# Optimization experiments

Hardware: AMD Instinct MI355X
Metric: run time of the kernel (lower is better)

Reference implementation:

```python
import jax, jax.numpy as jnp
import numpy as np
from functools import partial

NPOINT, NSAMPLE = 1024, 32
EPS = 1e-5

def setup_inputs() -> dict:
    key = jax.random.key(0)
    ks = jax.random.split(key, 16)
    B, N, C = 16, 4096, 64
    d = {
        "xyz": jax.random.normal(ks[0], (B, N, 3), jnp.float32),
        "points": jax.random.normal(ks[1], (B, N, C), jnp.float32),
    }
    chans = [67, 64, 64, 128]
    for i in range(3):
        cin, cout = chans[i], chans[i + 1]
        d[f"w{i+1}"] = jax.random.normal(ks[2 + i], (cout, cin), jnp.float32) * (1.0 / np.sqrt(cin))
        d[f"b{i+1}"] = jnp.zeros((cout,), jnp.float32)
        d[f"g{i+1}"] = jnp.ones((cout,), jnp.float32)
        d[f"be{i+1}"] = jnp.zeros((cout,), jnp.float32)
    return d

def farthest_point_sample(xyz, npoint):
    # xyz: (B, N, 3); deterministic start index 0 (torch code uses randint)
    B, N, _ = xyz.shape
    bidx = jnp.arange(B)

    def step(carry, _):
        distance, farthest = carry
        centroid = xyz[bidx, farthest]                       # (B, 3)
        dist = jnp.sum((xyz - centroid[:, None, :]) ** 2, -1)  # (B, N)
        distance = jnp.minimum(distance, dist)
        return (distance, jnp.argmax(distance, axis=1)), farthest

    init = (jnp.full((B, N), 1e10, xyz.dtype), jnp.zeros((B,), jnp.int32))
    _, centroids = jax.lax.scan(step, init, None, length=npoint)  # (npoint, B)
    return centroids.T                                            # (B, npoint)

def knn_group(nsample, xyz, new_xyz, points):
    # xyz: (B,N,3), new_xyz: (B,S,3), points: (B,N,C)
    # squared distances (same topk ordering as cdist)
    d2 = (jnp.sum(new_xyz ** 2, -1)[:, :, None]
          + jnp.sum(xyz ** 2, -1)[:, None, :]
          - 2.0 * jnp.einsum("bsd,bnd->bsn", new_xyz, xyz))     # (B,S,N)
    _, idx = jax.lax.top_k(-d2, nsample)                          # (B,S,K)

    gather = jax.vmap(lambda feats, i: feats[i])                  # per-batch fancy index
    grouped_xyz = gather(xyz, idx) - new_xyz[:, :, None, :]       # (B,S,K,3)
    grouped_pts = jnp.concatenate([grouped_xyz, gather(points, idx)], -1)  # (B,S,K,3+C)
    return grouped_xyz, grouped_pts

def mlp_layer(x, w, b, g, be):
    # 1x1 conv + BatchNorm (batch stats, training mode) + ReLU
    y = jnp.einsum("bskc,oc->bsko", x, w) + b
    mu = jnp.mean(y, axis=(0, 1, 2))
    var = jnp.var(y, axis=(0, 1, 2))
    y = (y - mu) * jax.lax.rsqrt(var + EPS) * g + be
    return jax.nn.relu(y)

def reference(xyz, points, w1, b1, g1, be1, w2, b2, g2, be2, w3, b3, g3, be3):
    centroids = farthest_point_sample(xyz, NPOINT)                    # (B,S)
    new_xyz = jnp.take_along_axis(xyz, centroids[:, :, None], axis=1)  # (B,S,3)
    _, x = knn_group(NSAMPLE, xyz, new_xyz, points)                   # (B,S,K,3+C)
    x = mlp_layer(x, w1, b1, g1, be1)
    x = mlp_layer(x, w2, b2, g2, be2)
    x = mlp_layer(x, w3, b3, g3, be3)
    new_points = jnp.max(x, axis=2)                                   # (B,S,mlp[-1])
    return new_xyz, new_points
```

## Files before the change

kernel.cpp:

```cpp
#include <hip/hip_runtime.h>

typedef unsigned int   uint;
typedef unsigned short ushort;
typedef unsigned long long u64;
typedef float f32x4 __attribute__((ext_vector_type(4)));
typedef short bf16x8 __attribute__((ext_vector_type(8)));
typedef uint  uint2v __attribute__((ext_vector_type(2)));

#define STR  88
#define STR1 104

__device__ __forceinline__ uint packbf2(float a, float b){
  uint ua=__float_as_uint(a); ua=(ua+0x7fffu+((ua>>16)&1u))>>16;
  uint ub=__float_as_uint(b); ub=(ub+0x7fffu+((ub>>16)&1u))>>16;
  return ua|(ub<<16);
}
__device__ __forceinline__ ushort bf1(float a){
  uint ua=__float_as_uint(a); return (ushort)((ua+0x7fffu+((ua>>16)&1u))>>16);
}

__global__ __launch_bounds__(256) void k_fps(const float* __restrict__ xyz,
                                             int* __restrict__ cent,
                                             float* __restrict__ oxyz,
                                             float* __restrict__ pxyz){
  __shared__ __align__(16) float sp[4096][4];
  __shared__ u64 rk[2][4];
  __shared__ int sel[1024];
  const int b = blockIdx.x, tid = threadIdx.x, lane=tid&63, wave=tid>>6;
  const float* xb = xyz + (long)b*4096*3;
  float px[16], py[16], pz[16], pd[16];
#pragma unroll
  for (int j=0;j<16;j++){
    int n = tid + 256*j;
    float x=xb[n*3], y=xb[n*3+1], z=xb[n*3+2];
    sp[n][0]=x; sp[n][1]=y; sp[n][2]=z; sp[n][3]=0.0f;
    px[j]=x; py[j]=y; pz[j]=z; pd[j]=1e10f;
  }
  if (tid==0) sel[0]=0;
  __syncthreads();
  int f = 0;
  for (int t=1;t<1024;t++){
    f32x4 c = *(const f32x4*)sp[f];
    float bv=-1.0f; int bi=0;
#pragma unroll
    for (int j=0;j<16;j++){
      int n = tid + 256*j;
      float dx=px[j]-c[0], dy=py[j]-c[1], dz=pz[j]-c[2];
      float d=__fadd_rn(__fadd_rn(__fmul_rn(dx,dx),__fmul_rn(dy,dy)),__fmul_rn(dz,dz));
      float mn=fminf(pd[j],d); pd[j]=mn;
      if (j==0){ bv=mn; bi=n; }
      else if (mn>bv){ bv=mn; bi=n; }
    }
    u64 key = ((u64)__float_as_uint(bv)<<32) | (uint)(~bi);
#pragma unroll
    for (int off=32;off;off>>=1){
      u64 ok=__shfl_xor(key,off);
      key = ok>key ? ok : key;
    }
    int par=t&1;
    if (lane==0) rk[par][wave]=key;
    __syncthreads();
    {
      u64 k0=rk[par][0], k1=rk[par][1], k2=rk[par][2], k3=rk[par][3];
      u64 ka = k0>k1?k0:k1;
      u64 kb = k2>k3?k2:k3;
      u64 kk = ka>kb?ka:kb;
      f = (int)(~(uint)kk) & 4095;
    }
    if (tid==0) sel[t]=f;
  }
  __syncthreads();
#pragma unroll
  for (int j=0;j<4;j++){
    int s = tid + 256*j;
    int n = sel[s];
    cent[b*1024+s]=n;
    f32x4 cf=*(const f32x4*)sp[n];
    oxyz[(b*1024+s)*3+0]=cf[0];
    oxyz[(b*1024+s)*3+1]=cf[1];
    oxyz[(b*1024+s)*3+2]=cf[2];
  }
#pragma unroll
  for (int j=0;j<16;j++){
    int n = tid + 256*j;
    *(f32x4*)(pxyz + ((long)b*4096+n)*4) = *(const f32x4*)sp[n];
  }
}

__global__ __launch_bounds__(256) void k_knn(const float* __restrict__ pxyz,
                                             const int* __restrict__ cent,
                                             ushort* __restrict__ kidx){
  const int bx=blockIdx.x, b=bx>>6, hc=bx&63;
  const int tid=threadIdx.x, lane=tid&63, wave=tid>>6;
  const f32x4* __restrict__ P = (const f32x4*)pxyz + (long)b*4096;
  const u64 SENT=~0ull;
  for (int qp=0; qp<2; qp++){
    int sA = hc*16 + wave*4 + qp*2;
    int sB = sA + 1;
    int qnA = cent[b*1024 + sA] & 4095;
    int qnB = cent[b*1024 + sB] & 4095;
    f32x4 QA = P[qnA], QB = P[qnB];
    double qxA=(double)QA[0], qyA=(double)QA[1], qzA=(double)QA[2];
    double qxB=(double)QB[0], qyB=(double)QB[1], qzB=(double)QB[2];
    u64 k1A=SENT, k2A=SENT, k1B=SENT, k2B=SENT;
#pragma unroll 4
    for (int j=0;j<64;j++){
      int n = lane + 64*j;
      f32x4 pt = P[n];
      double px=(double)pt[0], py=(double)pt[1], pz=(double)pt[2];
      double dxA=px-qxA, dyA=py-qyA, dzA=pz-qzA;
      double dxB=px-qxB, dyB=py-qyB, dzB=pz-qzB;
      double d2A = dxA*dxA + dyA*dyA + dzA*dzA;
      double d2B = dxB*dxB + dyB*dyB + dzB*dzB;
      u64 kdA = (((u64)__double_as_longlong(d2A)) & ~4095ull) | (uint)n;
      u64 kdB = (((u64)__double_as_longlong(d2B)) & ~4095ull) | (uint)n;
      if (kdA<k1A){ k2A=k1A; k1A=kdA; }
      else if (kdA<k2A){ k2A=kdA; }
      if (kdB<k1B){ k2B=k1B; k1B=kdB; }
      else if (kdB<k2B){ k2B=kdB; }
    }
    u64 removedA=0ull, removedB=0ull;
    ushort* outA = kidx + (b*1024 + sA)*32;
    ushort* outB = kidx + (b*1024 + sB)*32;
    for (int r=0;r<32;r++){
      u64 wkA=k1A, wkB=k1B;
#pragma unroll
      for (int off=32;off;off>>=1){
        u64 okA=__shfl_xor(wkA,off);
        u64 okB=__shfl_xor(wkB,off);
        wkA = okA<wkA ? okA : wkA;
        wkB = okB<wkB ? okB : wkB;
      }
      if (lane==0){ outA[r]=(ushort)(wkA & 4095u); outB[r]=(ushort)(wkB & 4095u); }
      if (wkA==k1A){
        removedA |= 1ull << (((uint)(k1A&4095u))>>6);
        if (k2A!=SENT){ k1A=k2A; k2A=SENT; }
        else {
          k1A=SENT; k2A=SENT;
#pragma unroll 4
          for (int j=0;j<64;j++){
            if ((removedA>>j)&1ull) continue;
            int n = lane + 64*j;
            f32x4 pt = P[n];
            double dx=(double)pt[0]-qxA, dy=(double)pt[1]-qyA, dz=(double)pt[2]-qzA;
            double d2 = dx*dx + dy*dy + dz*dz;
            u64 kd = (((u64)__double_as_longlong(d2)) & ~4095ull) | (uint)n;
            if (kd<k1A){ k2A=k1A; k1A=kd; }
            else if (kd<k2A){ k2A=kd; }
          }
        }
      }
      if (wkB==k1B){
        removedB |= 1ull << (((uint)(k1B&4095u))>>6);
        if (k2B!=SENT){ k1B=k2B; k2B=SENT; }
        else {
          k1B=SENT; k2B=SENT;
#pragma unroll 4
          for (int j=0;j<64;j++){
            if ((removedB>>j)&1ull) continue;
            int n = lane + 64*j;
            f32x4 pt = P[n];
            double dx=(double)pt[0]-qxB, dy=(double)pt[1]-qyB, dz=(double)pt[2]-qzB;
            double d2 = dx*dx + dy*dy + dz*dz;
            u64 kd = (((u64)__double_as_longlong(d2)) & ~4095ull) | (uint)n;
            if (kd<k1B){ k2B=k1B; k1B=kd; }
            else if (kd<k2B){ k2B=kd; }
          }
        }
      }
    }
  }
}

__global__ __launch_bounds__(256) void k_mlp1m(const float* __restrict__ xyz,
                                               const float* __restrict__ pts,
                                               const float* __restrict__ w1,
                                               const float* __restrict__ b1,
                                               const int* __restrict__ cent,
                                               const ushort* __restrict__ kidx,
                                               float* __restrict__ part,
                                               float* __restrict__ y){
  __shared__ __align__(16) ushort SA[128*STR1];
  __shared__ __align__(16) ushort SW[64*STR1];
  __shared__ float WRED[4*4*16*2];
  const int tid=threadIdx.x, bi=blockIdx.x;
  const int lane=tid&63, wave=tid>>6;
  const int lo16=lane&15, hi16=lane>>4;
  const long bN=(long)(bi>>6)*4096;

  for (int i=tid;i<64*96;i+=256){
    int r=i/96, c=i-r*96;
    float v = (c<64)? w1[r*67+3+c] : (c<67? w1[r*67+(c-64)] : 0.0f);
    SW[r*STR1+c]=bf1(v);
  }
  for (int i=tid;i<128*32;i+=256){
    int r=i>>5, c=64+(i&31);
    SA[r*STR1+c]=0;
  }
  const int ch4=(tid&15)*4, rb=(tid>>4)*8;
  float a1r[4];
#pragma unroll
  for (int nf=0;nf<4;nf++) a1r[nf]=b1[nf*16+lo16];
  float pss[4]={0.f,0.f,0.f,0.f}, pqq[4]={0.f,0.f,0.f,0.f};

  for (int t=0;t<4;t++){
    const long row0=(long)bi*512 + t*128;
    __syncthreads();
#pragma unroll
    for(int rr=0;rr<8;rr++){
      int r=rb+rr;
      long grow=row0+r;
      int n = kidx[grow] & 4095;
      f32x4 v=*(const f32x4*)(pts + (bN+n)*64 + ch4);
      uint2v pk; pk[0]=packbf2(v[0],v[1]); pk[1]=packbf2(v[2],v[3]);
      *(uint2v*)(SA+r*STR1+ch4)=pk;
    }
    if (tid<128){
      int r=tid;
      long grow=row0+r;
      int n = kidx[grow] & 4095;
      int q = cent[grow>>5] & 4095;
      const float* xp = xyz + (bN+n)*3;
      const float* qp = xyz + (bN+q)*3;
      SA[r*STR1+64]=bf1(xp[0]-qp[0]);
      SA[r*STR1+65]=bf1(xp[1]-qp[1]);
      SA[r*STR1+66]=bf1(xp[2]-qp[2]);
    }
    __syncthreads();
    const int mt=wave*32;
    f32x4 acc[2][4];
#pragma unroll
    for(int mf=0;mf<2;mf++)
#pragma unroll
      for(int nf=0;nf<4;nf++) acc[mf][nf]=(f32x4){0.f,0.f,0.f,0.f};
#pragma unroll
    for (int ks=0; ks<3; ks++){
      bf16x8 a0=*(const bf16x8*)(SA+(mt+lo16)*STR1    + ks*32 + hi16*8);
      bf16x8 a1f=*(const bf16x8*)(SA+(mt+16+lo16)*STR1 + ks*32 + hi16*8);
      bf16x8 b0=*(const bf16x8*)(SW+(lo16)*STR1     + ks*32 + hi16*8);
      bf16x8 b1f=*(const bf16x8*)(SW+(16+lo16)*STR1 + ks*32 + hi16*8);
      bf16x8 b2f=*(const bf16x8*)(SW+(32+lo16)*STR1 + ks*32 + hi16*8);
      bf16x8 b3f=*(const bf16x8*)(SW+(48+lo16)*STR1 + ks*32 + hi16*8);
      acc[0][0]=__builtin_amdgcn_mfma_f32_16x16x32_bf16(a0 ,b0 ,acc[0][0],0,0,0);
      acc[0][1]=__builtin_amdgcn_mfma_f32_16x16x32_bf16(a0 ,b1f,acc[0][1],0,0,0);
      acc[0][2]=__builtin_amdgcn_mfma_f32_16x16x32_bf16(a0 ,b2f,acc[0][2],0,0,0);
      acc[0][3]=__builtin_amdgcn_mfma_f32_16x16x32_bf16(a0 ,b3f,acc[0][3],0,0,0);
      acc[1][0]=__builtin_amdgcn_mfma_f32_16x16x32_bf16(a1f,b0 ,acc[1][0],0,0,0);
      acc[1][1]=__builtin_amdgcn_mfma_f32_16x16x32_bf16(a1f,b1f,acc[1][1],0,0,0);
      acc[1][2]=__builtin_amdgcn_mfma_f32_16x16x32_bf16(a1f,b2f,acc[1][2],0,0,0);
      acc[1][3]=__builtin_amdgcn_mfma_f32_16x16x32_bf16(a1f,b3f,acc[1][3],0,0,0);
    }
#pragma unroll
    for (int nf=0;nf<4;nf++){
#pragma unroll
      for (int mf=0;mf<2;mf++)
#pragma unroll
        for (int reg=0;reg<4;reg++){
          float d=acc[mf][nf][reg]+a1r[nf];
          long rr=row0+mt+mf*16+hi16*4+reg;
          y[rr*64 + nf*16+lo16]=d;
          pss[nf]+=d; pqq[nf]=fmaf(d,d,pqq[nf]);
        }
    }
  }
#pragma unroll
  for (int nf=0;nf<4;nf++){
    pss[nf]+=__shfl_xor(pss[nf],16); pss[nf]+=__shfl_xor(pss[nf],32);
    pqq[nf]+=__shfl_xor(pqq[nf],16); pqq[nf]+=__shfl_xor(pqq[nf],32);
  }
  if (lane<16){
#pragma unroll
    for (int nf=0;nf<4;nf++){
      WRED[((wave*4+nf)*16+lane)*2+0]=pss[nf];
      WRED[((wave*4+nf)*16+lane)*2+1]=pqq[nf];
    }
  }
  __syncthreads();
  if (tid<64){
    int ch=tid, nf=ch>>4, ci=ch&15;
    float s=0.f,q=0.f;
#pragma unroll
    for (int w=0;w<4;w++){ s+=WRED[((w*4+nf)*16+ci)*2]; q+=WRED[((w*4+nf)*16+ci)*2+1]; }
    part[(bi*64+ch)*2]=s; part[(bi*64+ch)*2+1]=q;
  }
}

__global__ __launch_bounds__(256) void k_mlp2m(const float* __restrict__ w2,
                                               const float* __restrict__ b2,
                                               const float* __restrict__ ab1,
                                               float* __restrict__ part,
                                               float* __restrict__ y){
  __shared__ __align__(16) ushort SA[128*STR];
  __shared__ __align__(16) ushort SW[64*STR];
  __shared__ float WRED[4*4*16*2];
  const int tid=threadIdx.x, bi=blockIdx.x;
  const int lane=tid&63, wave=tid>>6;
  const int lo16=lane&15, hi16=lane>>4;

  for (int i=tid;i<4096;i+=256){
    int r=i>>6, c=i&63;
    SW[r*STR+c]=bf1(w2[i]);
  }
  const int ch4=(tid&15)*4, rb=(tid>>4)*8;
  float a1[4],c1[4];
#pragma unroll
  for(int j=0;j<4;j++){ a1[j]=ab1[(ch4+j)*2]; c1[j]=ab1[(ch4+j)*2+1]; }
  float bbn[4];
#pragma unroll
  for (int nf=0;nf<4;nf++) bbn[nf]=b2[nf*16+lo16];
  float pss[4]={0.f,0.f,0.f,0.f}, pqq[4]={0.f,0.f,0.f,0.f};

  for (int t=0;t<4;t++){
    const long row0=(long)bi*512 + t*128;
    __syncthreads();
#pragma unroll
    for(int rr=0;rr<8;rr++){
      int r=rb+rr;
      f32x4 v=*(const f32x4*)(y+(row0+r)*64+ch4);
      float x0=fmaxf(fmaf(a1[0],v[0],c1[0]),0.f);
      float x1=fmaxf(fmaf(a1[1],v[1],c1[1]),0.f);
      float x2=fmaxf(fmaf(a1[2],v[2],c1[2]),0.f);
      float x3=fmaxf(fmaf(a1[3],v[3],c1[3]),0.f);
      uint2v pk; pk[0]=packbf2(x0,x1); pk[1]=packbf2(x2,x3);
      *(uint2v*)(SA+r*STR+ch4)=pk;
    }
    __syncthreads();
    const int mt=wave*32;
    f32x4 acc[2][4];
#pragma unroll
    for(int mf=0;mf<2;mf++)
#pragma unroll
      for(int nf=0;nf<4;nf++) acc[mf][nf]=(f32x4){0.f,0.f,0.f,0.f};
#pragma unroll
    for (int ks=0; ks<2; ks++){
      bf16x8 a0=*(const bf16x8*)(SA+(mt+lo16)*STR    + ks*32 + hi16*8);
      bf16x8 a1f=*(const bf16x8*)(SA+(mt+16+lo16)*STR + ks*32 + hi16*8);
      bf16x8 b0=*(const bf16x8*)(SW+(lo16)*STR     + ks*32 + hi16*8);
      bf16x8 b1=*(const bf16x8*)(SW+(16+lo16)*STR  + ks*32 + hi16*8);
      bf16x8 b2f=*(const bf16x8*)(SW+(32+lo16)*STR + ks*32 + hi16*8);
      bf16x8 b3f=*(const bf16x8*)(SW+(48+lo16)*STR + ks*32 + hi16*8);
      acc[0][0]=__builtin_amdgcn_mfma_f32_16x16x32_bf16(a0 ,b0 ,acc[0][0],0,0,0);
      acc[0][1]=__builtin_amdgcn_mfma_f32_16x16x32_bf16(a0 ,b1 ,acc[0][1],0,0,0);
      acc[0][2]=__builtin_amdgcn_mfma_f32_16x16x32_bf16(a0 ,b2f,acc[0][2],0,0,0);
      acc[0][3]=__builtin_amdgcn_mfma_f32_16x16x32_bf16(a0 ,b3f,acc[0][3],0,0,0);
      acc[1][0]=__builtin_amdgcn_mfma_f32_16x16x32_bf16(a1f,b0 ,acc[1][0],0,0,0);
      acc[1][1]=__builtin_amdgcn_mfma_f32_16x16x32_bf16(a1f,b1 ,acc[1][1],0,0,0);
      acc[1][2]=__builtin_amdgcn_mfma_f32_16x16x32_bf16(a1f,b2f,acc[1][2],0,0,0);
      acc[1][3]=__builtin_amdgcn_mfma_f32_16x16x32_bf16(a1f,b3f,acc[1][3],0,0,0);
    }
#pragma unroll
    for (int nf=0;nf<4;nf++){
#pragma unroll
      for (int mf=0;mf<2;mf++)
#pragma unroll
        for (int reg=0;reg<4;reg++){
          float d=acc[mf][nf][reg]+bbn[nf];
          long rr=row0+mt+mf*16+hi16*4+reg;
          y[rr*64 + nf*16+lo16]=d;
          pss[nf]+=d; pqq[nf]=fmaf(d,d,pqq[nf]);
        }
    }
  }
#pragma unroll
  for (int nf=0;nf<4;nf++){
    pss[nf]+=__shfl_xor(pss[nf],16); pss[nf]+=__shfl_xor(pss[nf],32);
    pqq[nf]+=__shfl_xor(pqq[nf],16); pqq[nf]+=__shfl_xor(pqq[nf],32);
  }
  if (lane<16){
#pragma unroll
    for (int nf=0;nf<4;nf++){
      WRED[((wave*4+nf)*16+lane)*2+0]=pss[nf];
      WRED[((wave*4+nf)*16+lane)*2+1]=pqq[nf];
    }
  }
  __syncthreads();
  if (tid<64){
    int ch=tid, nf=ch>>4, ci=ch&15;
    float s=0.f,q=0.f;
#pragma unroll
    for (int w=0;w<4;w++){ s+=WRED[((w*4+nf)*16+ci)*2]; q+=WRED[((w*4+nf)*16+ci)*2+1]; }
    part[(bi*64+ch)*2]=s; part[(bi*64+ch)*2+1]=q;
  }
}

__global__ __launch_bounds__(256) void k_mlp3m(const float* __restrict__ w3,
                                               const float* __restrict__ b3,
                                               const float* __restrict__ ab2,
                                               float* __restrict__ part,
                                               const float* __restrict__ y,
                                               float* __restrict__ mx){
  __shared__ __align__(16) ushort SA[128*STR];
  __shared__ __align__(16) ushort SW[128*STR];
  __shared__ float WRED[4*8*16*2];
  const int tid=threadIdx.x, bi=blockIdx.x;
  const int lane=tid&63, wave=tid>>6;
  const int lo16=lane&15, hi16=lane>>4;

  for (int i=tid;i<8192;i+=256){
    int r=i>>6, c=i&63;
    SW[r*STR+c]=bf1(w3[i]);
  }
  const int ch4=(tid&15)*4, rb=(tid>>4)*8;
  float a2[4],c2[4];
#pragma unroll
  for(int j=0;j<4;j++){ a2[j]=ab2[(ch4+j)*2]; c2[j]=ab2[(ch4+j)*2+1]; }
  float bbn[8];
#pragma unroll
  for (int nf=0;nf<8;nf++) bbn[nf]=b3[nf*16+lo16];
  float pss[8], pqq[8];
#pragma unroll
  for (int nf=0;nf<8;nf++){ pss[nf]=0.f; pqq[nf]=0.f; }

  for (int t=0;t<4;t++){
    const long row0=(long)bi*512 + t*128;
    __syncthreads();
#pragma unroll
    for(int rr=0;rr<8;rr++){
      int r=rb+rr;
      f32x4 v=*(const f32x4*)(y+(row0+r)*64+ch4);
      float x0=fmaxf(fmaf(a2[0],v[0],c2[0]),0.f);
      float x1=fmaxf(fmaf(a2[1],v[1],c2[1]),0.f);
      float x2=fmaxf(fmaf(a2[2],v[2],c2[2]),0.f);
      float x3=fmaxf(fmaf(a2[3],v[3],c2[3]),0.f);
      uint2v pk; pk[0]=packbf2(x0,x1); pk[1]=packbf2(x2,x3);
      *(uint2v*)(SA+r*STR+ch4)=pk;
    }
    __syncthreads();
    const int mt=wave*32;
    f32x4 acc[2][8];
#pragma unroll
    for(int mf=0;mf<2;mf++)
#pragma unroll
      for(int nf=0;nf<8;nf++) acc[mf][nf]=(f32x4){0.f,0.f,0.f,0.f};
#pragma unroll
    for (int ks=0; ks<2; ks++){
      bf16x8 a0=*(const bf16x8*)(SA+(mt+lo16)*STR    + ks*32 + hi16*8);
      bf16x8 a1f=*(const bf16x8*)(SA+(mt+16+lo16)*STR + ks*32 + hi16*8);
#pragma unroll
      for (int nf=0;nf<8;nf++){
        bf16x8 bv=*(const bf16x8*)(SW+(nf*16+lo16)*STR + ks*32 + hi16*8);
        acc[0][nf]=__builtin_amdgcn_mfma_f32_16x16x32_bf16(a0 ,bv,acc[0][nf],0,0,0);
        acc[1][nf]=__builtin_amdgcn_mfma_f32_16x16x32_bf16(a1f,bv,acc[1][nf],0,0,0);
      }
    }
    float vmx[8];
#pragma unroll
    for (int nf=0;nf<8;nf++) vmx[nf]=-3.0e38f;
#pragma unroll
    for (int nf=0;nf<8;nf++){
#pragma unroll
      for (int mf=0;mf<2;mf++)
#pragma unroll
        for (int reg=0;reg<4;reg++){
          float d=acc[mf][nf][reg]+bbn[nf];
          pss[nf]+=d; pqq[nf]=fmaf(d,d,pqq[nf]);
          vmx[nf]=fmaxf(vmx[nf],d);
        }
    }
#pragma unroll
    for (int nf=0;nf<8;nf++){
      vmx[nf]=fmaxf(vmx[nf],__shfl_xor(vmx[nf],16));
      vmx[nf]=fmaxf(vmx[nf],__shfl_xor(vmx[nf],32));
    }
    {
      long sg = (long)bi*16 + t*4 + wave;
      if (lane<16){
#pragma unroll
        for (int nf=0;nf<8;nf++) mx[sg*128 + nf*16 + lane]=vmx[nf];
      }
    }
  }
#pragma unroll
  for (int nf=0;nf<8;nf++){
    pss[nf]+=__shfl_xor(pss[nf],16); pss[nf]+=__shfl_xor(pss[nf],32);
    pqq[nf]+=__shfl_xor(pqq[nf],16); pqq[nf]+=__shfl_xor(pqq[nf],32);
  }
  if (lane<16){
#pragma unroll
    for (int nf=0;nf<8;nf++){
      WRED[((wave*8+nf)*16+lane)*2+0]=pss[nf];
      WRED[((wave*8+nf)*16+lane)*2+1]=pqq[nf];
    }
  }
  __syncthreads();
  if (tid<128){
    int ch=tid, nf=ch>>4, ci=ch&15;
    float s=0.f,q=0.f;
#pragma unroll
    for (int w=0;w<4;w++){ s+=WRED[((w*8+nf)*16+ci)*2]; q+=WRED[((w*8+nf)*16+ci)*2+1]; }
    part[(bi*128+ch)*2]=s; part[(bi*128+ch)*2+1]=q;
  }
}

__global__ void k_red(const float* __restrict__ part,
                      const float* __restrict__ gam,
                      const float* __restrict__ bet,
                      float* __restrict__ ab, int nch, int nblk){
  __shared__ float red[4][128][2];
  const int tid=threadIdx.x, ch=tid%nch, seg=tid/nch;
  float s=0.f,q=0.f;
  for (int i=seg;i<nblk;i+=4){ s+=part[(i*nch+ch)*2]; q+=part[(i*nch+ch)*2+1]; }
  red[seg][ch][0]=s; red[seg][ch][1]=q;
  __syncthreads();
  if (seg==0){
    s=red[0][ch][0]+red[1][ch][0]+red[2][ch][0]+red[3][ch][0];
    q=red[0][ch][1]+red[1][ch][1]+red[2][ch][1]+red[3][ch][1];
    float mu=s*(1.0f/524288.0f);
    float var=q*(1.0f/524288.0f)-mu*mu;
    var=fmaxf(var,0.0f);
    float a=gam[ch]/sqrtf(var+1e-5f);
    float c=bet[ch]-mu*a;
    ab[ch*2]=a; ab[ch*2+1]=c;
  }
}

__global__ __launch_bounds__(256) void k_out(const float* __restrict__ mx,
                                             const float* __restrict__ ab3,
                                             float* __restrict__ onp){
  int i = (blockIdx.x*256 + threadIdx.x)*4;
  int ch = i & 127;
  f32x4 v = *(const f32x4*)(mx+i);
  f32x4 r;
  r[0]=fmaxf(fmaf(ab3[(ch+0)*2], v[0], ab3[(ch+0)*2+1]), 0.0f);
  r[1]=fmaxf(fmaf(ab3[(ch+1)*2], v[1], ab3[(ch+1)*2+1]), 0.0f);
  r[2]=fmaxf(fmaf(ab3[(ch+2)*2], v[2], ab3[(ch+2)*2+1]), 0.0f);
  r[3]=fmaxf(fmaf(ab3[(ch+3)*2], v[3], ab3[(ch+3)*2+1]), 0.0f);
  *(f32x4*)(onp+i)=r;
}

extern "C" void kernel_launch(void* const* d_in, const int* in_sizes, int n_in,
                              void* d_out, int out_size, void* d_ws, size_t ws_size,
                              hipStream_t stream){
  const float* xyz=(const float*)d_in[0];
  const float* pts=(const float*)d_in[1];
  const float* w1 =(const float*)d_in[2];
  const float* b1 =(const float*)d_in[3];
  const float* g1 =(const float*)d_in[4];
  const float* be1=(const float*)d_in[5];
  const float* w2 =(const float*)d_in[6];
  const float* b2 =(const float*)d_in[7];
  const float* g2 =(const float*)d_in[8];
  const float* be2=(const float*)d_in[9];
  const float* w3 =(const float*)d_in[10];
  const float* b3 =(const float*)d_in[11];
  const float* g3 =(const float*)d_in[12];
  const float* be3=(const float*)d_in[13];
  char* ws=(char*)d_ws;
  int*    cent=(int*)(ws);
  ushort* kidx=(ushort*)(ws+  65536);
  float*  p   =(float*)(ws+ 1114112);
  float*  ab1 =(float*)(ws+ 2162688);
  float*  ab2 =(float*)(ws+ 2163200);
  float*  ab3 =(float*)(ws+ 2163712);
  float*  mx  =(float*)(ws+ 2164736);
  float*  pxyz=(float*)(ws+11534336);
  float*  y   =(float*)(ws+16777216);
  float* oxyz=(float*)d_out;
  float* onp =oxyz + 16*1024*3;

  k_fps<<<16, 256, 0, stream>>>(xyz, cent, oxyz, pxyz);
  k_knn<<<1024, 256, 0, stream>>>(pxyz, cent, kidx);
  k_mlp1m<<<1024, 256, 0, stream>>>(xyz, pts, w1, b1, cent, kidx, p, y);
  k_red<<<1, 256, 0, stream>>>(p, g1, be1, ab1, 64, 1024);
  k_mlp2m<<<1024, 256, 0, stream>>>(w2, b2, ab1, p, y);
  k_red<<<1, 256, 0, stream>>>(p, g2, be2, ab2, 64, 1024);
  k_mlp3m<<<1024, 256, 0, stream>>>(w3, b3, ab2, p, y, mx);
  k_red<<<1, 512, 0, stream>>>(p, g3, be3, ab3, 128, 1024);
  k_out<<<2048, 256, 0, stream>>>(mx, ab3, onp);
}
```

Measured before the change: 1.695 ms.

## Fuse FPS and KNN into one kernel with flag-based streaming overlap

Merges the farthest-point-sampling and KNN kernels into one launch. The first 16 blocks run FPS at raised priority and publish centroids in chunks of 128 through release flags, while the remaining blocks spin on acquire flags and start KNN for each chunk as soon as it is ready. The KNN work is also split to one query per wave instead of two. The goal is to hide KNN behind the long serial FPS loop. The risks are spin-wait scheduling problems, such as FPS blocks not being resident when waiting blocks fill the device, plus an extra memset and a large LDS allocation in every block, which lowers KNN occupancy.

```diff
diff --git a/kernel.cpp b/kernel.cpp
--- a/kernel.cpp
+++ b/kernel.cpp
@@ -19,152 +19,131 @@
   uint ua=__float_as_uint(a); return (ushort)((ua+0x7fffu+((ua>>16)&1u))>>16);
 }
 
-__global__ __launch_bounds__(256) void k_fps(const float* __restrict__ xyz,
-                                             int* __restrict__ cent,
-                                             float* __restrict__ oxyz,
-                                             float* __restrict__ pxyz){
-  __shared__ __align__(16) float sp[4096][4];
-  __shared__ u64 rk[2][4];
-  __shared__ int sel[1024];
-  const int b = blockIdx.x, tid = threadIdx.x, lane=tid&63, wave=tid>>6;
-  const float* xb = xyz + (long)b*4096*3;
-  float px[16], py[16], pz[16], pd[16];
-#pragma unroll
-  for (int j=0;j<16;j++){
-    int n = tid + 256*j;
-    float x=xb[n*3], y=xb[n*3+1], z=xb[n*3+2];
-    sp[n][0]=x; sp[n][1]=y; sp[n][2]=z; sp[n][3]=0.0f;
-    px[j]=x; py[j]=y; pz[j]=z; pd[j]=1e10f;
-  }
-  if (tid==0) sel[0]=0;
-  __syncthreads();
-  int f = 0;
-  for (int t=1;t<1024;t++){
-    f32x4 c = *(const f32x4*)sp[f];
-    float bv=-1.0f; int bi=0;
+__global__ __launch_bounds__(256) void k_fk(const float* __restrict__ xyz,
+                                            int* __restrict__ cent,
+                                            float* __restrict__ oxyz,
+                                            float* __restrict__ pxyz,
+                                            ushort* __restrict__ kidx,
+                                            int* __restrict__ flags){
+  __shared__ __align__(16) char LU[69760];
+  const int bid=blockIdx.x, tid=threadIdx.x, lane=tid&63, wave=tid>>6;
+  const u64 SENT=~0ull;
+
+  if (bid < 16){
+    __builtin_amdgcn_s_setprio(1);
+    float (*sp)[4] = (float(*)[4])LU;
+    u64* rk  = (u64*)(LU + 65536);
+    int* sel = (int*)(LU + 65600);
+    const int b = bid;
+    const float* xb = xyz + (long)b*4096*3;
+    float px[16], py[16], pz[16], pd[16];
 #pragma unroll
     for (int j=0;j<16;j++){
       int n = tid + 256*j;
-      float dx=px[j]-c[0], dy=py[j]-c[1], dz=pz[j]-c[2];
-      float d=__fadd_rn(__fadd_rn(__fmul_rn(dx,dx),__fmul_rn(dy,dy)),__fmul_rn(dz,dz));
-      float mn=fminf(pd[j],d); pd[j]=mn;
-      if (j==0){ bv=mn; bi=n; }
-      else if (mn>bv){ bv=mn; bi=n; }
-    }
-    u64 key = ((u64)__float_as_uint(bv)<<32) | (uint)(~bi);
-#pragma unroll
-    for (int off=32;off;off>>=1){
-      u64 ok=__shfl_xor(key,off);
-      key = ok>key ? ok : key;
-    }
-    int par=t&1;
-    if (lane==0) rk[par][wave]=key;
-    __syncthreads();
-    {
-      u64 k0=rk[par][0], k1=rk[par][1], k2=rk[par][2], k3=rk[par][3];
-      u64 ka = k0>k1?k0:k1;
-      u64 kb = k2>k3?k2:k3;
-      u64 kk = ka>kb?ka:kb;
-      f = (int)(~(uint)kk) & 4095;
-    }
-    if (tid==0) sel[t]=f;
-  }
-  __syncthreads();
-#pragma unroll
-  for (int j=0;j<4;j++){
-    int s = tid + 256*j;
-    int n = sel[s];
-    cent[b*1024+s]=n;
-    f32x4 cf=*(const f32x4*)sp[n];
-    oxyz[(b*1024+s)*3+0]=cf[0];
-    oxyz[(b*1024+s)*3+1]=cf[1];
-    oxyz[(b*1024+s)*3+2]=cf[2];
-  }
-#pragma unroll
-  for (int j=0;j<16;j++){
-    int n = tid + 256*j;
-    *(f32x4*)(pxyz + ((long)b*4096+n)*4) = *(const f32x4*)sp[n];
-  }
-}
-
-__global__ __launch_bounds__(256) void k_knn(const float* __restrict__ pxyz,
-                                             const int* __restrict__ cent,
-                                             ushort* __restrict__ kidx){
-  const int bx=blockIdx.x, b=bx>>6, hc=bx&63;
-  const int tid=threadIdx.x, lane=tid&63, wave=tid>>6;
-  const f32x4* __restrict__ P = (const f32x4*)pxyz + (long)b*4096;
-  const u64 SENT=~0ull;
-  for (int qp=0; qp<2; qp++){
-    int sA = hc*16 + wave*4 + qp*2;
-    int sB = sA + 1;
-    int qnA = cent[b*1024 + sA] & 4095;
-    int qnB = cent[b*1024 + sB] & 4095;
-    f32x4 QA = P[qnA], QB = P[qnB];
-    double qxA=(double)QA[0], qyA=(double)QA[1], qzA=(double)QA[2];
-    double qxB=(double)QB[0], qyB=(double)QB[1], qzB=(double)QB[2];
-    u64 k1A=SENT, k2A=SENT, k1B=SENT, k2B=SENT;
+      float x=xb[n*3], y=xb[n*3+1], z=xb[n*3+2];
+      sp[n][0]=x; sp[n][1]=y; sp[n][2]=z; sp[n][3]=0.0f;
+      px[j]=x; py[j]=y; pz[j]=z; pd[j]=1e10f;
+      *(f32x4*)(pxyz + ((long)b*4096+n)*4) = (f32x4){x,y,z,0.0f};
+    }
+    __threadfence();
+    if (tid==0){ sel[0]=0; cent[b*1024]=0; }
+    __syncthreads();
+    int f = 0;
+    for (int t=1;t<1024;t++){
+      f32x4 c = *(const f32x4*)sp[f];
+      float bv=-1.0f; int bi=0;
+#pragma unroll
+      for (int j=0;j<16;j++){
+        int n = tid + 256*j;
+        float dx=px[j]-c[0], dy=py[j]-c[1], dz=pz[j]-c[2];
+        float d=__fadd_rn(__fadd_rn(__fmul_rn(dx,dx),__fmul_rn(dy,dy)),__fmul_rn(dz,dz));
+        float mn=fminf(pd[j],d); pd[j]=mn;
+        if (j==0){ bv=mn; bi=n; }
+        else if (mn>bv){ bv=mn; bi=n; }
+      }
+      u64 key = ((u64)__float_as_uint(bv)<<32) | (uint)(~bi);
+#pragma unroll
+      for (int off=32;off;off>>=1){
+        u64 ok=__shfl_xor(key,off);
+        key = ok>key ? ok : key;
+      }
+      int par=t&1;
+      if (lane==0) rk[par*4+wave]=key;
+      __syncthreads();
+      {
+        u64 k0=rk[par*4+0], k1=rk[par*4+1], k2=rk[par*4+2], k3=rk[par*4+3];
+        u64 ka = k0>k1?k0:k1;
+        u64 kb = k2>k3?k2:k3;
+        u64 kk = ka>kb?ka:kb;
+        f = (int)(~(uint)kk) & 4095;
+      }
+      if (tid==0){
+        sel[t]=f;
+        cent[b*1024+t]=f;
+        if ((t&127)==127)
+          __hip_atomic_store(&flags[b*8+(t>>7)], 1, __ATOMIC_RELEASE, __HIP_MEMORY_SCOPE_AGENT);
+      }
+    }
+    __syncthreads();
+#pragma unroll
+    for (int j=0;j<4;j++){
+      int s = tid + 256*j;
+      int n = sel[s];
+      f32x4 cf=*(const f32x4*)sp[n];
+      oxyz[(b*1024+s)*3+0]=cf[0];
+      oxyz[(b*1024+s)*3+1]=cf[1];
+      oxyz[(b*1024+s)*3+2]=cf[2];
+    }
+  } else {
+    const int u = bid-16;
+    const int b = u>>8, qb = (u&255)*4;
+    if (tid==0){
+      int st = (qb+3)>>7;
+      while (__hip_atomic_load(&flags[b*8+st], __ATOMIC_ACQUIRE, __HIP_MEMORY_SCOPE_AGENT)==0)
+        __builtin_amdgcn_s_sleep(64);
+    }
+    __syncthreads();
+    const f32x4* __restrict__ P = (const f32x4*)pxyz + (long)b*4096;
+    const int s = qb + wave;
+    int qn = cent[b*1024 + s] & 4095;
+    f32x4 Q = P[qn];
+    double qx=(double)Q[0], qy=(double)Q[1], qz=(double)Q[2];
+    u64 k1=SENT, k2=SENT;
 #pragma unroll 4
     for (int j=0;j<64;j++){
       int n = lane + 64*j;
       f32x4 pt = P[n];
-      double px=(double)pt[0], py=(double)pt[1], pz=(double)pt[2];
-      double dxA=px-qxA, dyA=py-qyA, dzA=pz-qzA;
-      double dxB=px-qxB, dyB=py-qyB, dzB=pz-qzB;
-      double d2A = dxA*dxA + dyA*dyA + dzA*dzA;
-      double d2B = dxB*dxB + dyB*dyB + dzB*dzB;
-      u64 kdA = (((u64)__double_as_longlong(d2A)) & ~4095ull) | (uint)n;
-      u64 kdB = (((u64)__double_as_longlong(d2B)) & ~4095ull) | (uint)n;
-      if (kdA<k1A){ k2A=k1A; k1A=kdA; }
-      else if (kdA<k2A){ k2A=kdA; }
-      if (kdB<k1B){ k2B=k1B; k1B=kdB; }
-      else if (kdB<k2B){ k2B=kdB; }
-    }
-    u64 removedA=0ull, removedB=0ull;
-    ushort* outA = kidx + (b*1024 + sA)*32;
-    ushort* outB = kidx + (b*1024 + sB)*32;
+      double dx=(double)pt[0]-qx, dy=(double)pt[1]-qy, dz=(double)pt[2]-qz;
+      double d2 = dx*dx + dy*dy + dz*dz;
+      u64 kd = (((u64)__double_as_longlong(d2)) & ~4095ull) | (uint)n;
+      if (kd<k1){ k2=k1; k1=kd; }
+      else if (kd<k2){ k2=kd; }
+    }
+    u64 removed=0ull;
+    ushort* outp = kidx + (b*1024 + s)*32;
     for (int r=0;r<32;r++){
-      u64 wkA=k1A, wkB=k1B;
+      u64 wk=k1;
 #pragma unroll
       for (int off=32;off;off>>=1){
-        u64 okA=__shfl_xor(wkA,off);
-        u64 okB=__shfl_xor(wkB,off);
-        wkA = okA<wkA ? okA : wkA;
-        wkB = okB<wkB ? okB : wkB;
-      }
-      if (lane==0){ outA[r]=(ushort)(wkA & 4095u); outB[r]=(ushort)(wkB & 4095u); }
-      if (wkA==k1A){
-        removedA |= 1ull << (((uint)(k1A&4095u))>>6);
-        if (k2A!=SENT){ k1A=k2A; k2A=SENT; }
+        u64 ok=__shfl_xor(wk,off);
+        wk = ok<wk ? ok : wk;
+      }
+      if (lane==0) outp[r]=(ushort)(wk & 4095u);
+      if (wk==k1){
+        removed |= 1ull << (((uint)(k1&4095u))>>6);
+        if (k2!=SENT){ k1=k2; k2=SENT; }
         else {
-          k1A=SENT; k2A=SENT;
+          k1=SENT; k2=SENT;
 #pragma unroll 4
           for (int j=0;j<64;j++){
-            if ((removedA>>j)&1ull) continue;
+            if ((removed>>j)&1ull) continue;
             int n = lane + 64*j;
             f32x4 pt = P[n];
-            double dx=(double)pt[0]-qxA, dy=(double)pt[1]-qyA, dz=(double)pt[2]-qzA;
+            double dx=(double)pt[0]-qx, dy=(double)pt[1]-qy, dz=(double)pt[2]-qz;
             double d2 = dx*dx + dy*dy + dz*dz;
             u64 kd = (((u64)__double_as_longlong(d2)) & ~4095ull) | (uint)n;
-            if (kd<k1A){ k2A=k1A; k1A=kd; }
-            else if (kd<k2A){ k2A=kd; }
-          }
-        }
-      }
-      if (wkB==k1B){
-        removedB |= 1ull << (((uint)(k1B&4095u))>>6);
-        if (k2B!=SENT){ k1B=k2B; k2B=SENT; }
-        else {
-          k1B=SENT; k2B=SENT;
-#pragma unroll 4
-          for (int j=0;j<64;j++){
-            if ((removedB>>j)&1ull) continue;
-            int n = lane + 64*j;
-            f32x4 pt = P[n];
-            double dx=(double)pt[0]-qxB, dy=(double)pt[1]-qyB, dz=(double)pt[2]-qzB;
-            double d2 = dx*dx + dy*dy + dz*dz;
-            u64 kd = (((u64)__double_as_longlong(d2)) & ~4095ull) | (uint)n;
-            if (kd<k1B){ k2B=k1B; k1B=kd; }
-            else if (kd<k2B){ k2B=kd; }
+            if (kd<k1){ k2=k1; k1=kd; }
+            else if (kd<k2){ k2=kd; }
           }
         }
       }
@@ -554,12 +533,13 @@
   float*  ab3 =(float*)(ws+ 2163712);
   float*  mx  =(float*)(ws+ 2164736);
   float*  pxyz=(float*)(ws+11534336);
+  int*    flags=(int*)(ws+15728640);
   float*  y   =(float*)(ws+16777216);
   float* oxyz=(float*)d_out;
   float* onp =oxyz + 16*1024*3;
 
-  k_fps<<<16, 256, 0, stream>>>(xyz, cent, oxyz, pxyz);
-  k_knn<<<1024, 256, 0, stream>>>(pxyz, cent, kidx);
+  hipMemsetAsync(flags, 0, 512, stream);
+  k_fk<<<4112, 256, 0, stream>>>(xyz, cent, oxyz, pxyz, kidx, flags);
   k_mlp1m<<<1024, 256, 0, stream>>>(xyz, pts, w1, b1, cent, kidx, p, y);
   k_red<<<1, 256, 0, stream>>>(p, g1, be1, ab1, 64, 1024);
   k_mlp2m<<<1024, 256, 0, stream>>>(w2, b2, ab1, p, y);
```

After: 1.881 ms. 11.0% more time.
